# Performance work log

Measured on AMD Instinct MI355X. Metric: run time of the kernel, lower is better.

Reference implementation:

```python
import jax, jax.numpy as jnp
import numpy as np

B, NC, CH, HF, WF = 2, 6, 256, 32, 88
N, CIN = 100000, 128
VOXEL_SIZE = jnp.array([0.075, 0.075, 0.2], dtype=jnp.float32)
PC_MIN = jnp.array([-54.0, -54.0, -5.0], dtype=jnp.float32)
DOWNSAMPLE = 8.0
DMIN, DMAX = 1.0, 60.0


def setup_inputs() -> dict:
    key = jax.random.key(0)
    ks = jax.random.split(key, 12)
    # voxel coords: (batch, z, y, x), batch column sorted to match the
    # original per-batch-loop concatenation order
    b = jnp.repeat(jnp.arange(B, dtype=jnp.int32), N // B)
    x = jax.random.randint(ks[0], (N,), 0, 1440, dtype=jnp.int32)
    y = jax.random.randint(ks[1], (N,), 0, 1440, dtype=jnp.int32)
    z = jax.random.randint(ks[2], (N,), 0, 40, dtype=jnp.int32)
    voxel_coords = jnp.stack([b, z, y, x], axis=1)
    voxel_features = jax.random.normal(ks[3], (N, CIN), dtype=jnp.float32)
    img_feats = jax.random.normal(ks[4], (B, NC, CH, HF, WF), dtype=jnp.float32)
    # pinhole intrinsics for a 704x256 image
    K = jnp.array([[500.0, 0.0, 352.0], [0.0, 500.0, 128.0], [0.0, 0.0, 1.0]], dtype=jnp.float32)
    intrins = K + 0.01 * jax.random.normal(ks[5], (B, NC, 3, 3), dtype=jnp.float32)
    post_rots = 0.5 * jnp.eye(3, dtype=jnp.float32) + 0.001 * jax.random.normal(ks[6], (B, NC, 3, 3), dtype=jnp.float32)
    post_trans = 0.01 * jax.random.normal(ks[7], (B, NC, 3), dtype=jnp.float32)
    # bda: near-identity 4x4
    bda = jnp.tile(jnp.eye(4, dtype=jnp.float32), (B, 1, 1))
    bda = bda.at[:, :3, :3].add(0.01 * jax.random.normal(ks[8], (B, 3, 3), dtype=jnp.float32))
    bda = bda.at[:, :3, 3].set(0.1 * jax.random.normal(ks[9], (B, 3), dtype=jnp.float32))
    # lidar->cam: standard axis permutation (x->z) so depth is positive for half the scene
    R = jnp.array([[0.0, -1.0, 0.0], [0.0, 0.0, -1.0], [1.0, 0.0, 0.0]], dtype=jnp.float32)
    l2c = jnp.tile(jnp.eye(4, dtype=jnp.float32), (B, NC, 1, 1))
    l2c = l2c.at[..., :3, :3].set(R + 0.01 * jax.random.normal(ks[10], (B, NC, 3, 3), dtype=jnp.float32))
    l2c = l2c.at[..., :3, 3].set(0.1 * jax.random.normal(ks[11], (B, NC, 3), dtype=jnp.float32))
    W = 0.02 * jax.random.normal(jax.random.fold_in(key, 99), (CIN, CH), dtype=jnp.float32)
    return dict(voxel_features=voxel_features, voxel_coords=voxel_coords, img_feats=img_feats,
                intrins=intrins, post_rots=post_rots, post_trans=post_trans, bda=bda,
                lidar2cam=l2c, W=W)


def reference(voxel_features, voxel_coords, img_feats, intrins, post_rots, post_trans, bda, lidar2cam, W):
    bidx = voxel_coords[:, 0]
    # voxel index (x,y,z) -> metric lidar coords
    p = voxel_coords[:, jnp.array([3, 2, 1])].astype(jnp.float32) * VOXEL_SIZE + PC_MIN  # [N,3]
    # undo bda augmentation: (p - t) @ inv(R).T
    binv = jnp.linalg.inv(bda[:, :3, :3])  # [B,3,3]
    pcam = jnp.einsum('nj,nij->ni', p - bda[bidx, :3, 3], binv[bidx])  # [N,3]
    # lidar2img = cam2img @ lidar2cam.T (faithful to original, incl. full 4x4 transpose)
    cam2img = jnp.tile(jnp.eye(4, dtype=intrins.dtype), (B, NC, 1, 1)).at[..., :3, :3].set(intrins)
    L = cam2img @ jnp.swapaxes(lidar2cam, -1, -2)  # [B,NC,4,4]
    Lv = L[bidx]  # [N,NC,4,4]
    pimg = jnp.einsum('nj,ncij->nci', pcam, Lv[:, :, :3, :3]) + Lv[:, :, :3, 3]  # [N,NC,3]
    pimg = jnp.concatenate([pimg[..., :2] / pimg[..., 2:3], pimg[..., 2:3]], axis=-1)
    pimg = jnp.einsum('ncj,ncij->nci', pimg, post_rots[bidx]) + post_trans[bidx]
    # gather_img_feature: round/clip + masked gather, scatter into zeros == multiply by mask
    coor = jnp.round(pimg[..., :2] / DOWNSAMPLE)
    depth = pimg[..., 2]
    mask = ((coor[..., 0] >= 0) & (coor[..., 0] < WF) & (coor[..., 1] >= 0) & (coor[..., 1] < HF)
            & (depth < DMAX) & (depth >= DMIN))  # [N,NC]
    xi = jnp.clip(coor[..., 0].astype(jnp.int32), 0, WF - 1)
    yi = jnp.clip(coor[..., 1].astype(jnp.int32), 0, HF - 1)
    cams = jnp.arange(NC)[None, :]
    g = img_feats[bidx[:, None], cams, :, yi, xi]  # [N,NC,CH]
    g = g * mask[..., None].astype(g.dtype)
    # sum over cameras, then Linear(256 -> CIN, no bias)
    img_voxel = jnp.einsum('nc,oc->no', g.sum(axis=1), W)  # [N,CIN]
    out_feats = jnp.concatenate([voxel_features, img_voxel], axis=0)  # [2N,CIN]
    out_coords = jnp.concatenate([voxel_coords, voxel_coords], axis=0)  # [2N,4]
    return out_feats, out_coords
```

## Files before the change

kernel.cpp:

```cpp
#include <hip/hip_runtime.h>
#include <math.h>

#define BB   2
#define NCAM 6
#define CH   256
#define HF   32
#define WF   88
#define NV   100000
#define CIN  128
#define VPB  16
#define SGP  (CH + 4)

typedef __attribute__((ext_vector_type(8))) short short8;
typedef __attribute__((ext_vector_type(4))) float f32x4;

static __device__ inline short f2bf(float f) {
    union { float f; unsigned u; } v; v.f = f;
    unsigned r = (v.u + 0x7fffu + ((v.u >> 16) & 1u)) >> 16;
    return (short)r;
}

__global__ void precompute_params(const float* __restrict__ intrins,
                                  const float* __restrict__ post_rots,
                                  const float* __restrict__ post_trans,
                                  const float* __restrict__ bda,
                                  const float* __restrict__ l2c,
                                  double* __restrict__ params)
{
    int t = threadIdx.x;
    if (t >= BB * NCAM) return;
    int b = t / NCAM;

    const float* Bm = bda + b * 16;
    double a00 = Bm[0], a01 = Bm[1], a02 = Bm[2],  tx = Bm[3];
    double a10 = Bm[4], a11 = Bm[5], a12 = Bm[6],  ty = Bm[7];
    double a20 = Bm[8], a21 = Bm[9], a22 = Bm[10], tz = Bm[11];

    double det = a00*(a11*a22 - a12*a21) - a01*(a10*a22 - a12*a20) + a02*(a10*a21 - a11*a20);
    double id  = 1.0 / det;
    double inv[3][3];
    inv[0][0] =  (a11*a22 - a12*a21) * id;
    inv[0][1] = -(a01*a22 - a02*a21) * id;
    inv[0][2] =  (a01*a12 - a02*a11) * id;
    inv[1][0] = -(a10*a22 - a12*a20) * id;
    inv[1][1] =  (a00*a22 - a02*a20) * id;
    inv[1][2] = -(a00*a12 - a02*a10) * id;
    inv[2][0] =  (a10*a21 - a11*a20) * id;
    inv[2][1] = -(a00*a21 - a01*a20) * id;
    inv[2][2] =  (a00*a11 - a01*a10) * id;

    const float* In = intrins + t * 9;
    const float* Lc = l2c + t * 16;

    double M3[3][3];
    #pragma unroll
    for (int i = 0; i < 3; i++)
        #pragma unroll
        for (int j = 0; j < 3; j++)
            M3[i][j] = (double)In[i*3+0] * (double)Lc[j*4+0]
                     + (double)In[i*3+1] * (double)Lc[j*4+1]
                     + (double)In[i*3+2] * (double)Lc[j*4+2];

    double M[3][3];
    #pragma unroll
    for (int i = 0; i < 3; i++)
        #pragma unroll
        for (int j = 0; j < 3; j++)
            M[i][j] = M3[i][0]*inv[0][j] + M3[i][1]*inv[1][j] + M3[i][2]*inv[2][j];

    double* P = params + t * 24;
    #pragma unroll
    for (int i = 0; i < 3; i++)
        #pragma unroll
        for (int j = 0; j < 3; j++)
            P[i*3+j] = M[i][j];
    #pragma unroll
    for (int i = 0; i < 3; i++)
        P[9+i] = -(M[i][0]*tx + M[i][1]*ty + M[i][2]*tz);
    #pragma unroll
    for (int i = 0; i < 9; i++) P[12+i] = (double)post_rots[t*9 + i];
    #pragma unroll
    for (int i = 0; i < 3; i++) P[21+i] = (double)post_trans[t*3 + i];
}

__global__ void convert_W(const float* __restrict__ W, short* __restrict__ Wbf)
{
    int chunk = blockIdx.x;
    int l = threadIdx.x;
    int nt = chunk >> 3, kk = chunk & 7;
    int n = nt * 16 + (l & 15);
    int k = kk * 32 + (l >> 4) * 8;
    short v[8];
    #pragma unroll
    for (int j = 0; j < 8; j++) v[j] = f2bf(W[n * CH + k + j]);
    *(short8*)(Wbf + ((size_t)chunk * 64 + l) * 8) = *(short8*)v;
}

__global__ __launch_bounds__(256) void transpose_img(const float* __restrict__ img,
                                                     float* __restrict__ imgT)
{
    __shared__ float tile[32][89];
    int bid = blockIdx.x;
    int cg  = bid & 7;
    int y   = (bid >> 3) & 31;
    int bc  = bid >> 8;
    int t   = threadIdx.x;

    const float* src = img + ((size_t)(bc * CH + cg * 32)) * (HF * WF) + y * WF;
    #pragma unroll
    for (int i = 0; i < 11; i++) {
        int lin = i * 256 + t;
        int ch  = lin / 88;
        int x   = lin - ch * 88;
        tile[ch][x] = src[(size_t)ch * (HF * WF) + x];
    }
    __syncthreads();
    float* dst = imgT + ((size_t)(bc * HF + y) * WF) * CH + cg * 32;
    #pragma unroll
    for (int j = 0; j < 11; j++) {
        int lin = j * 256 + t;
        int x   = lin >> 5;
        int ch  = lin & 31;
        dst[(size_t)x * CH + ch] = tile[ch][x];
    }
}

template <bool TRANS>
__global__ __launch_bounds__(256) void fused_gather_mm(
    const float*  __restrict__ vf,
    const int*    __restrict__ coords,
    const float*  __restrict__ img,
    const double* __restrict__ params,
    const short*  __restrict__ Wbf,
    float*        __restrict__ out)
{
    const int t  = threadIdx.x;
    const int n0 = blockIdx.x * VPB;

    {
        const float4* vf4 = (const float4*)vf;
        float4*       o4  = (float4*)out;
        int base = n0 * (CIN / 4);
        o4[base + t]       = vf4[base + t];
        o4[base + 256 + t] = vf4[base + 256 + t];
    }
    if (t < VPB * 4) {
        int gi = n0 * 4 + t;
        float cv = (float)coords[gi];
        const size_t cb = (size_t)2 * NV * CIN;
        out[cb + gi]                  = cv;
        out[cb + (size_t)NV * 4 + gi] = cv;
    }

    __shared__ int   pofs[VPB][NCAM];
    __shared__ float sg[VPB][SGP];
    __shared__ __align__(16) short aFrag[8 * 64 * 8];

    if (t < VPB * NCAM) {
        int vi = t / NCAM, c = t - vi * NCAM;
        int n  = n0 + vi;
        int b  = coords[n * 4 + 0];
        int zi = coords[n * 4 + 1];
        int yi = coords[n * 4 + 2];
        int xi = coords[n * 4 + 3];
        double px = (double)xi * (double)0.075f + (-54.0);
        double py = (double)yi * (double)0.075f + (-54.0);
        double pz = (double)zi * (double)0.2f   + (-5.0);
        const double* P = params + (b * NCAM + c) * 24;
        double X = P[0]*px + P[1]*py + P[2]*pz + P[9];
        double Y = P[3]*px + P[4]*py + P[5]*pz + P[10];
        double Z = P[6]*px + P[7]*py + P[8]*pz + P[11];
        double u = X / Z;
        double v = Y / Z;
        double q0 = P[12]*u + P[13]*v + P[14]*Z + P[21];
        double q1 = P[15]*u + P[16]*v + P[17]*Z + P[22];
        double q2 = P[18]*u + P[19]*v + P[20]*Z + P[23];
        double cx = rint(q0 * 0.125);
        double cy = rint(q1 * 0.125);
        bool m = (cx >= 0.0) && (cx < (double)WF) && (cy >= 0.0) && (cy < (double)HF)
              && (q2 < 60.0) && (q2 >= 1.0);
        int o = -1;
        if (m) {
            int ix = (int)cx, iy = (int)cy;
            if (TRANS) o = ((b * NCAM + c) * HF + iy) * WF + ix;
            else       o = (b * NCAM + c) * (CH * HF * WF) + iy * WF + ix;
        }
        pofs[vi][c] = o;
    }
    __syncthreads();

    #pragma unroll
    for (int vi = 0; vi < VPB; vi++) {
        float g = 0.0f;
        #pragma unroll
        for (int c = 0; c < NCAM; c++) {
            int o = pofs[vi][c];
            if (o >= 0) {
                if (TRANS) g += img[(size_t)o * CH + t];
                else       g += img[(size_t)o + (size_t)t * (HF * WF)];
            }
        }
        sg[vi][t] = g;
    }
    __syncthreads();

    #pragma unroll
    for (int p = 0; p < 2; p++) {
        int c2 = t + p * 256;
        int kk = c2 >> 6;
        int l  = c2 & 63;
        int m  = l & 15;
        int k  = kk * 32 + (l >> 4) * 8;
        short tmp[8];
        #pragma unroll
        for (int j = 0; j < 8; j++) tmp[j] = f2bf(sg[m][k + j]);
        *(short8*)(aFrag + c2 * 8) = *(short8*)tmp;
    }
    __syncthreads();

    {
        const int w    = t >> 6;
        const int lane = t & 63;
        f32x4 acc0 = {0.f, 0.f, 0.f, 0.f};
        f32x4 acc1 = {0.f, 0.f, 0.f, 0.f};
        const short8* Bf = (const short8*)Wbf;
        #pragma unroll
        for (int kk = 0; kk < 8; kk++) {
            short8 a  = *(const short8*)(aFrag + (kk * 64 + lane) * 8);
            short8 b0 = Bf[((2 * w)     * 8 + kk) * 64 + lane];
            short8 b1 = Bf[((2 * w + 1) * 8 + kk) * 64 + lane];
            acc0 = __builtin_amdgcn_mfma_f32_16x16x32_bf16(a, b0, acc0, 0, 0, 0);
            acc1 = __builtin_amdgcn_mfma_f32_16x16x32_bf16(a, b1, acc1, 0, 0, 0);
        }
        float* oiv = out + (size_t)NV * CIN;
        int col = lane & 15, rq = lane >> 4;
        #pragma unroll
        for (int r = 0; r < 4; r++) {
            int n = n0 + rq * 4 + r;
            oiv[(size_t)n * CIN + (2 * w)     * 16 + col] = acc0[r];
            oiv[(size_t)n * CIN + (2 * w + 1) * 16 + col] = acc1[r];
        }
    }
}

extern "C" void kernel_launch(void* const* d_in, const int* in_sizes, int n_in,
                              void* d_out, int out_size, void* d_ws, size_t ws_size,
                              hipStream_t stream)
{
    const float* vf      = (const float*)d_in[0];
    const int*   coords  = (const int*)d_in[1];
    const float* img     = (const float*)d_in[2];
    const float* intrins = (const float*)d_in[3];
    const float* prots   = (const float*)d_in[4];
    const float* ptrans  = (const float*)d_in[5];
    const float* bda     = (const float*)d_in[6];
    const float* l2c     = (const float*)d_in[7];
    const float* W       = (const float*)d_in[8];
    float* out = (float*)d_out;

    double* params = (double*)d_ws;
    const size_t wbf_off  = 4096;
    const size_t wbf_sz   = (size_t)8 * 8 * 64 * 8 * sizeof(short);
    const size_t imgT_off = wbf_off + wbf_sz;
    const size_t needed   = imgT_off + (size_t)BB * NCAM * CH * HF * WF * sizeof(float);

    short* Wbf = (short*)((char*)d_ws + wbf_off);

    precompute_params<<<1, 64, 0, stream>>>(intrins, prots, ptrans, bda, l2c, params);
    convert_W<<<64, 64, 0, stream>>>(W, Wbf);

    if (ws_size >= needed) {
        float* imgT = (float*)((char*)d_ws + imgT_off);
        transpose_img<<<BB * NCAM * HF * 8, 256, 0, stream>>>(img, imgT);
        fused_gather_mm<true><<<NV / VPB, 256, 0, stream>>>(vf, coords, imgT, params, Wbf, out);
    } else {
        fused_gather_mm<false><<<NV / VPB, 256, 0, stream>>>(vf, coords, img, params, Wbf, out);
    }
}
```

Measured before the change: 238.2 us.

## Store transposed image features as bf16 and merge param/W prep kernels

The transpose kernel now writes the channel-last image copy in bf16 packed pairs instead of fp32. The gather loop reads two channels per thread as one 32-bit load and sums 8 voxels per half-block. This halves the transpose write traffic and the random-gather read traffic. The param and W conversion kernels are fused into one launch, and the smem-to-bf16 fragment packing uses float4 reads. Rounding the gathered features to bf16 before summing adds a small precision loss.

```diff
diff --git a/kernel.cpp b/kernel.cpp
--- a/kernel.cpp
+++ b/kernel.cpp
@@ -20,13 +20,28 @@
     return (short)r;
 }
 
-__global__ void precompute_params(const float* __restrict__ intrins,
-                                  const float* __restrict__ post_rots,
-                                  const float* __restrict__ post_trans,
-                                  const float* __restrict__ bda,
-                                  const float* __restrict__ l2c,
-                                  double* __restrict__ params)
+__global__ void prep_params_w(const float* __restrict__ intrins,
+                              const float* __restrict__ post_rots,
+                              const float* __restrict__ post_trans,
+                              const float* __restrict__ bda,
+                              const float* __restrict__ l2c,
+                              const float* __restrict__ W,
+                              double* __restrict__ params,
+                              short*  __restrict__ Wbf)
 {
+    if (blockIdx.x > 0) {
+        int chunk = blockIdx.x - 1;
+        int l = threadIdx.x;
+        int nt = chunk >> 3, kk = chunk & 7;
+        int n = nt * 16 + (l & 15);
+        int k = kk * 32 + (l >> 4) * 8;
+        short v[8];
+        #pragma unroll
+        for (int j = 0; j < 8; j++) v[j] = f2bf(W[n * CH + k + j]);
+        *(short8*)(Wbf + ((size_t)chunk * 64 + l) * 8) = *(short8*)v;
+        return;
+    }
+
     int t = threadIdx.x;
     if (t >= BB * NCAM) return;
     int b = t / NCAM;
@@ -83,21 +98,8 @@
     for (int i = 0; i < 3; i++) P[21+i] = (double)post_trans[t*3 + i];
 }
 
-__global__ void convert_W(const float* __restrict__ W, short* __restrict__ Wbf)
-{
-    int chunk = blockIdx.x;
-    int l = threadIdx.x;
-    int nt = chunk >> 3, kk = chunk & 7;
-    int n = nt * 16 + (l & 15);
-    int k = kk * 32 + (l >> 4) * 8;
-    short v[8];
-    #pragma unroll
-    for (int j = 0; j < 8; j++) v[j] = f2bf(W[n * CH + k + j]);
-    *(short8*)(Wbf + ((size_t)chunk * 64 + l) * 8) = *(short8*)v;
-}
-
 __global__ __launch_bounds__(256) void transpose_img(const float* __restrict__ img,
-                                                     float* __restrict__ imgT)
+                                                     unsigned short* __restrict__ imgT)
 {
     __shared__ float tile[32][89];
     int bid = blockIdx.x;
@@ -115,13 +117,18 @@
         tile[ch][x] = src[(size_t)ch * (HF * WF) + x];
     }
     __syncthreads();
-    float* dst = imgT + ((size_t)(bc * HF + y) * WF) * CH + cg * 32;
-    #pragma unroll
-    for (int j = 0; j < 11; j++) {
-        int lin = j * 256 + t;
-        int x   = lin >> 5;
-        int ch  = lin & 31;
-        dst[(size_t)x * CH + ch] = tile[ch][x];
+
+    unsigned short* dst = imgT + ((size_t)(bc * HF + y) * WF) * CH + cg * 32;
+    #pragma unroll
+    for (int j = 0; j < 6; j++) {
+        int lin2 = j * 256 + t;
+        if (j == 5 && t >= 128) break;
+        int x  = lin2 >> 4;
+        int cp = lin2 & 15;
+        unsigned short lo = (unsigned short)f2bf(tile[2 * cp][x]);
+        unsigned short hi = (unsigned short)f2bf(tile[2 * cp + 1][x]);
+        unsigned int pk = (unsigned int)lo | ((unsigned int)hi << 16);
+        *(unsigned int*)(dst + (size_t)x * CH + 2 * cp) = pk;
     }
 }
 
@@ -129,7 +136,7 @@
 __global__ __launch_bounds__(256) void fused_gather_mm(
     const float*  __restrict__ vf,
     const int*    __restrict__ coords,
-    const float*  __restrict__ img,
+    const void*   __restrict__ imgv,
     const double* __restrict__ params,
     const short*  __restrict__ Wbf,
     float*        __restrict__ out)
@@ -189,18 +196,40 @@
     }
     __syncthreads();
 
-    #pragma unroll
-    for (int vi = 0; vi < VPB; vi++) {
-        float g = 0.0f;
-        #pragma unroll
-        for (int c = 0; c < NCAM; c++) {
-            int o = pofs[vi][c];
-            if (o >= 0) {
-                if (TRANS) g += img[(size_t)o * CH + t];
-                else       g += img[(size_t)o + (size_t)t * (HF * WF)];
+    if (TRANS) {
+        const unsigned short* imgT = (const unsigned short*)imgv;
+        int u  = t & 127;
+        int vh = t >> 7;
+        #pragma unroll
+        for (int s = 0; s < VPB / 2; s++) {
+            int vi = vh * (VPB / 2) + s;
+            float g0 = 0.0f, g1 = 0.0f;
+            #pragma unroll
+            for (int c = 0; c < NCAM; c++) {
+                int o = pofs[vi][c];
+                if (o >= 0) {
+                    unsigned int pk = *(const unsigned int*)(imgT + (size_t)o * CH + 2 * u);
+                    union { unsigned int u; float f; } a, b;
+                    a.u = pk << 16;
+                    b.u = pk & 0xffff0000u;
+                    g0 += a.f;
+                    g1 += b.f;
+                }
             }
-        }
-        sg[vi][t] = g;
+            *(float2*)&sg[vi][2 * u] = make_float2(g0, g1);
+        }
+    } else {
+        const float* img = (const float*)imgv;
+        #pragma unroll
+        for (int vi = 0; vi < VPB; vi++) {
+            float g = 0.0f;
+            #pragma unroll
+            for (int c = 0; c < NCAM; c++) {
+                int o = pofs[vi][c];
+                if (o >= 0) g += img[(size_t)o + (size_t)t * (HF * WF)];
+            }
+            sg[vi][t] = g;
+        }
     }
     __syncthreads();
 
@@ -211,9 +240,11 @@
         int l  = c2 & 63;
         int m  = l & 15;
         int k  = kk * 32 + (l >> 4) * 8;
+        float4 v0 = *(const float4*)&sg[m][k];
+        float4 v1 = *(const float4*)&sg[m][k + 4];
         short tmp[8];
-        #pragma unroll
-        for (int j = 0; j < 8; j++) tmp[j] = f2bf(sg[m][k + j]);
+        tmp[0] = f2bf(v0.x); tmp[1] = f2bf(v0.y); tmp[2] = f2bf(v0.z); tmp[3] = f2bf(v0.w);
+        tmp[4] = f2bf(v1.x); tmp[5] = f2bf(v1.y); tmp[6] = f2bf(v1.z); tmp[7] = f2bf(v1.w);
         *(short8*)(aFrag + c2 * 8) = *(short8*)tmp;
     }
     __syncthreads();
@@ -262,15 +293,14 @@
     const size_t wbf_off  = 4096;
     const size_t wbf_sz   = (size_t)8 * 8 * 64 * 8 * sizeof(short);
     const size_t imgT_off = wbf_off + wbf_sz;
-    const size_t needed   = imgT_off + (size_t)BB * NCAM * CH * HF * WF * sizeof(float);
+    const size_t needed   = imgT_off + (size_t)BB * NCAM * HF * WF * CH * sizeof(unsigned short);
 
     short* Wbf = (short*)((char*)d_ws + wbf_off);
 
-    precompute_params<<<1, 64, 0, stream>>>(intrins, prots, ptrans, bda, l2c, params);
-    convert_W<<<64, 64, 0, stream>>>(W, Wbf);
+    prep_params_w<<<65, 64, 0, stream>>>(intrins, prots, ptrans, bda, l2c, W, params, Wbf);
 
     if (ws_size >= needed) {
-        float* imgT = (float*)((char*)d_ws + imgT_off);
+        unsigned short* imgT = (unsigned short*)((char*)d_ws + imgT_off);
         transpose_img<<<BB * NCAM * HF * 8, 256, 0, stream>>>(img, imgT);
         fused_gather_mm<true><<<NV / VPB, 256, 0, stream>>>(vf, coords, imgT, params, Wbf, out);
     } else {
```

After: 222.3 us. 6.6% less time.
